# Kernel tuning notes

Measured on AMD Instinct MI355X. Metric: run time of the kernel, lower is better.

Reference implementation:

```python
import jax, jax.numpy as jnp
import numpy as np

CUTOFF = 5.0
NUM_RADIAL = 8
MAX_DEGREE = 3
NUM_EMB = 64
N_ELEM = 83
N_ATOMS = 20000
N_NBR = 32

# degree index for each of the 16 (l,m) components: l=0(x1),1(x3),2(x5),3(x7)
_LM_TO_L = np.repeat(np.arange(MAX_DEGREE + 1), [1, 3, 5, 7])


def jinclike(x, num, limit):
    """Jinc-like radial basis, f_n version (arXiv:1907.02374). x: (...,) -> (..., num)."""
    i = jnp.arange(num, dtype=jnp.float32)
    factor1 = (2.0 ** 0.5) * jnp.pi / (limit ** 1.5)
    factor2 = ((-1.0) ** i) * (i + 1.0) * (i + 2.0) / jnp.hypot(i + 1.0, i + 2.0)
    x = x[..., None]
    return factor1 * factor2 * (jnp.sinc(x / limit * (i + 1.0)) + jnp.sinc(x / limit * (i + 2.0)))


def sph_harm16(u):
    """Real spherical harmonics up to l=3, Racah normalization (Y00=1),
    spherical order m=-l..l (cartesian_order=False). u: (..., 3) unit vectors -> (..., 16)."""
    x, y, z = u[..., 0], u[..., 1], u[..., 2]
    s3, s6, s10, s15 = 3.0 ** 0.5, 6.0 ** 0.5, 10.0 ** 0.5, 15.0 ** 0.5
    one = jnp.ones_like(x)
    comps = [
        one,                                   # l=0
        y, z, x,                               # l=1, m=-1,0,1
        s3 * x * y, s3 * y * z, 0.5 * (3.0 * z * z - 1.0), s3 * x * z, 0.5 * s3 * (x * x - y * y),  # l=2
        0.25 * s10 * y * (3.0 * x * x - y * y), s15 * x * y * z, 0.25 * s6 * y * (5.0 * z * z - 1.0),
        0.5 * z * (5.0 * z * z - 3.0),
        0.25 * s6 * x * (5.0 * z * z - 1.0), 0.5 * s15 * z * (x * x - y * y), 0.25 * s10 * x * (x * x - 3.0 * y * y),  # l=3
    ]
    return jnp.stack(comps, axis=-1)


def setup_inputs() -> dict:
    key = jax.random.key(0)
    k1, k2, k3, k4, k5, k6 = jax.random.split(key, 6)
    neighbour_displacements = 1.5 * jax.random.normal(k1, (N_ATOMS, N_NBR, 3), dtype=jnp.float32)
    Z_j = jax.random.randint(k2, (N_ATOMS, N_NBR), 0, N_ELEM, dtype=jnp.int32)
    embed_table = jax.random.normal(k3, (N_ELEM, NUM_EMB), dtype=jnp.float32)
    dense_w = jax.random.normal(k4, (NUM_EMB, NUM_RADIAL), dtype=jnp.float32) / (NUM_EMB ** 0.5)
    dense_b = 0.01 * jax.random.normal(k5, (NUM_RADIAL,), dtype=jnp.float32)
    tensor_w = jax.random.normal(k6, (MAX_DEGREE + 1, NUM_RADIAL), dtype=jnp.float32)
    return {"neighbour_displacements": neighbour_displacements, "Z_j": Z_j,
            "embed_table": embed_table, "dense_w": dense_w, "dense_b": dense_b,
            "tensor_w": tensor_w}


def reference(neighbour_displacements, Z_j, embed_table, dense_w, dense_b, tensor_w):
    # radial x angular basis expansion: (N, K, 16, 8)
    norm = jnp.linalg.norm(neighbour_displacements, axis=-1)            # (N, K)
    u = neighbour_displacements / norm[..., None]                        # unit vectors
    rbf = jinclike(norm, NUM_RADIAL, CUTOFF)                             # (N, K, 8)
    sh = sph_harm16(u)                                                   # (N, K, 16)
    basis = sh[..., :, None] * rbf[..., None, :]                         # (N, K, 16, 8)

    # species embedding -> dense transform to num_radial channels (scalar, l=0 features)
    emb = embed_table[Z_j]                                               # (N, K, 64)
    t = emb @ dense_w + dense_b                                          # (N, K, 8)

    # CG tensor product with a scalar (l=0) left input collapses exactly to a
    # per-degree weighted elementwise product: y[lm,f] = w[l(lm),f] * t[f] * basis[lm,f]
    wexp = tensor_w[_LM_TO_L]                                            # (16, 8)
    y = wexp * t[..., None, :] * basis                                   # (N, K, 16, 8)

    y = y.at[..., 0, :].add(t)

    return y[..., None, :, :].astype(jnp.float32)
```

## Files before the change

### kernel.cpp

```cpp
#include <hip/hip_runtime.h>
#include <math.h>

#define N_ATOMS   20000
#define N_NBR     32
#define NBR_TOTAL (N_ATOMS * N_NBR)
#define N_ELEM    83
#define NUM_EMB   64
#define NUM_RAD   8

__global__ __launch_bounds__(256) void sarb_kernel(
    const float* __restrict__ disp,
    const int*   __restrict__ Zj,
    const float* __restrict__ embed,
    const float* __restrict__ dw,
    const float* __restrict__ db,
    const float* __restrict__ tw,
    float* __restrict__ out)
{
    __shared__ float Fl[N_ELEM * NUM_RAD];
    __shared__ float lds[256 * 33];

    const int tid = threadIdx.x;

    for (int i = tid; i < N_ELEM * NUM_RAD; i += 256) {
        int z = i >> 3, f = i & 7;
        float acc = db[f];
        const float* er = embed + z * NUM_EMB;
        for (int e = 0; e < NUM_EMB; ++e)
            acc = fmaf(er[e], dw[e * 8 + f], acc);
        Fl[i] = acc;
    }
    __syncthreads();

    const int n = blockIdx.x * 256 + tid;
    const float dx = disp[n * 3 + 0];
    const float dy = disp[n * 3 + 1];
    const float dz = disp[n * 3 + 2];
    const int   z  = Zj[n];

    const float r2  = dx * dx + dy * dy + dz * dz;
    const float nrm = sqrtf(r2);
    const float inv = 1.0f / nrm;
    const float x = dx * inv, y = dy * inv, zu = dz * inv;

    const float s3 = 1.7320508075688772f, s6 = 2.449489742783178f;
    const float s10 = 3.1622776601683795f, s15 = 3.872983346207417f;
    const float x2 = x * x, y2 = y * y, z2 = zu * zu;
    const float xy = x * y, yz = y * zu, xz = x * zu;

    const int base = tid * 33;
    lds[base + 0]  = 1.0f;
    lds[base + 1]  = y;
    lds[base + 2]  = zu;
    lds[base + 3]  = x;
    lds[base + 4]  = s3 * xy;
    lds[base + 5]  = s3 * yz;
    lds[base + 6]  = 0.5f * (3.0f * z2 - 1.0f);
    lds[base + 7]  = s3 * xz;
    lds[base + 8]  = 0.5f * s3 * (x2 - y2);
    lds[base + 9]  = 0.25f * s10 * y * (3.0f * x2 - y2);
    lds[base + 10] = s15 * xy * zu;
    lds[base + 11] = 0.25f * s6 * y * (5.0f * z2 - 1.0f);
    lds[base + 12] = 0.5f * zu * (5.0f * z2 - 3.0f);
    lds[base + 13] = 0.25f * s6 * x * (5.0f * z2 - 1.0f);
    lds[base + 14] = 0.5f * s15 * zu * (x2 - y2);
    lds[base + 15] = 0.25f * s10 * x * (x2 - 3.0f * y2);

    const float a = 0.6283185307179586f * nrm;
    float sv[9];
    {
        const float s1  = sinf(a);
        const float c2  = 2.0f * cosf(a);
        const float inva = 1.0f / a;
        const float invk[9] = {1.0f, 0.5f, 0.33333333f, 0.25f, 0.2f,
                               0.16666667f, 0.14285714f, 0.125f, 0.11111111f};
        float sprev = 0.0f, scur = s1;
        #pragma unroll
        for (int k = 0; k < 9; ++k) {
            sv[k] = scur * inva * invk[k];
            float snext = c2 * scur - sprev;
            sprev = scur; scur = snext;
        }
        if (a < 1e-12f) {
            #pragma unroll
            for (int k = 0; k < 9; ++k) sv[k] = 1.0f;
        }
    }
    #pragma unroll
    for (int i = 0; i < 8; ++i) {
        const float ip1 = (float)(i + 1), ip2 = (float)(i + 2);
        float f2 = ip1 * ip2 / sqrtf(ip1 * ip1 + ip2 * ip2);
        if (i & 1) f2 = -f2;
        const float rbf = 0.3973835397f * f2 * (sv[i] + sv[i + 1]);
        const float tf  = Fl[z * 8 + i];
        lds[base + 16 + i] = tf * rbf;
        lds[base + 24 + i] = tf;
    }
    __syncthreads();

    const int chunk = tid & 31;
    const int lm = chunk >> 1;
    const int fh = (chunk & 1) * 4;
    const int l  = (lm > 0) + (lm > 3) + (lm > 8);
    const float4 wv = *reinterpret_cast<const float4*>(tw + l * 8 + fh);

    float4* outv = reinterpret_cast<float4*>(out) + (size_t)blockIdx.x * 8192;
    const int nb0 = tid >> 5;
    #pragma unroll
    for (int k = 0; k < 32; ++k) {
        const int nb = k * 8 + nb0;
        const int b  = nb * 33;
        const float s = lds[b + lm];
        const float g0 = lds[b + 16 + fh + 0];
        const float g1 = lds[b + 16 + fh + 1];
        const float g2 = lds[b + 16 + fh + 2];
        const float g3 = lds[b + 16 + fh + 3];
        float4 r;
        r.x = wv.x * s * g0;
        r.y = wv.y * s * g1;
        r.z = wv.z * s * g2;
        r.w = wv.w * s * g3;
        if (lm == 0) {
            r.x += lds[b + 24 + fh + 0];
            r.y += lds[b + 24 + fh + 1];
            r.z += lds[b + 24 + fh + 2];
            r.w += lds[b + 24 + fh + 3];
        }
        outv[k * 256 + tid] = r;
    }
}

extern "C" void kernel_launch(void* const* d_in, const int* in_sizes, int n_in,
                              void* d_out, int out_size, void* d_ws, size_t ws_size,
                              hipStream_t stream) {
    const float* disp  = (const float*)d_in[0];
    const int*   Zj    = (const int*)  d_in[1];
    const float* embed = (const float*)d_in[2];
    const float* dw    = (const float*)d_in[3];
    const float* db    = (const float*)d_in[4];
    const float* tw    = (const float*)d_in[5];
    float* out = (float*)d_out;

    sarb_kernel<<<dim3(NBR_TOTAL / 256), dim3(256), 0, stream>>>(
        disp, Zj, embed, dw, db, tw, out);
}
```

Before: 352.0 us.

## Precompute species-to-radial table in separate kernel and streamline output stage

Moves the 83x8 embedding-dense table computation out of every block into a tiny prologue kernel writing to workspace. Each block then only copies the table into padded LDS. The row stride is padded to 34 so LDS reads can be 8-byte vectors. The l=0 residual is folded into a precomputed slot, which removes the branch in the store loop. The change also uses fast __sincosf and nontemporal stores for the large output. The risks are an extra kernel launch and the lower precision of the fast sincos.

```diff
diff --git a/kernel.cpp b/kernel.cpp
--- a/kernel.cpp
+++ b/kernel.cpp
@@ -6,36 +6,46 @@
 #define NBR_TOTAL (N_ATOMS * N_NBR)
 #define N_ELEM    83
 #define NUM_EMB   64
-#define NUM_RAD   8
+#define ROWW      34
+
+typedef float f32x4 __attribute__((ext_vector_type(4)));
+
+__global__ __launch_bounds__(256) void f_table_kernel(
+    const float* __restrict__ embed, const float* __restrict__ dw,
+    const float* __restrict__ db, float* __restrict__ F)
+{
+    const int i = blockIdx.x * 256 + threadIdx.x;
+    if (i < N_ELEM * 8) {
+        const int z = i >> 3, f = i & 7;
+        float acc = db[f];
+        const float* er = embed + z * NUM_EMB;
+        #pragma unroll 8
+        for (int e = 0; e < NUM_EMB; ++e)
+            acc = fmaf(er[e], dw[e * 8 + f], acc);
+        F[i] = acc;
+    }
+}
 
 __global__ __launch_bounds__(256) void sarb_kernel(
     const float* __restrict__ disp,
     const int*   __restrict__ Zj,
-    const float* __restrict__ embed,
-    const float* __restrict__ dw,
-    const float* __restrict__ db,
     const float* __restrict__ tw,
+    const float* __restrict__ Fg,
     float* __restrict__ out)
 {
-    __shared__ float Fl[N_ELEM * NUM_RAD];
-    __shared__ float lds[256 * 33];
+    __shared__ float Fl[N_ELEM * 9 + 1];
+    __shared__ __align__(16) float lds[256 * ROWW];
 
     const int tid = threadIdx.x;
 
-    for (int i = tid; i < N_ELEM * NUM_RAD; i += 256) {
-        int z = i >> 3, f = i & 7;
-        float acc = db[f];
-        const float* er = embed + z * NUM_EMB;
-        for (int e = 0; e < NUM_EMB; ++e)
-            acc = fmaf(er[e], dw[e * 8 + f], acc);
-        Fl[i] = acc;
-    }
+    for (int i = tid; i < N_ELEM * 8; i += 256)
+        Fl[(i >> 3) * 9 + (i & 7)] = Fg[i];
     __syncthreads();
 
     const int n = blockIdx.x * 256 + tid;
-    const float dx = disp[n * 3 + 0];
-    const float dy = disp[n * 3 + 1];
-    const float dz = disp[n * 3 + 2];
+    const float dx = disp[3 * n + 0];
+    const float dy = disp[3 * n + 1];
+    const float dz = disp[3 * n + 2];
     const int   z  = Zj[n];
 
     const float r2  = dx * dx + dy * dy + dz * dz;
@@ -48,37 +58,38 @@
     const float x2 = x * x, y2 = y * y, z2 = zu * zu;
     const float xy = x * y, yz = y * zu, xz = x * zu;
 
-    const int base = tid * 33;
-    lds[base + 0]  = 1.0f;
-    lds[base + 1]  = y;
-    lds[base + 2]  = zu;
-    lds[base + 3]  = x;
-    lds[base + 4]  = s3 * xy;
-    lds[base + 5]  = s3 * yz;
-    lds[base + 6]  = 0.5f * (3.0f * z2 - 1.0f);
-    lds[base + 7]  = s3 * xz;
-    lds[base + 8]  = 0.5f * s3 * (x2 - y2);
-    lds[base + 9]  = 0.25f * s10 * y * (3.0f * x2 - y2);
-    lds[base + 10] = s15 * xy * zu;
-    lds[base + 11] = 0.25f * s6 * y * (5.0f * z2 - 1.0f);
-    lds[base + 12] = 0.5f * zu * (5.0f * z2 - 3.0f);
-    lds[base + 13] = 0.25f * s6 * x * (5.0f * z2 - 1.0f);
-    lds[base + 14] = 0.5f * s15 * zu * (x2 - y2);
-    lds[base + 15] = 0.25f * s10 * x * (x2 - 3.0f * y2);
+    float* row = lds + tid * ROWW;
+    row[0]  = 1.0f;
+    row[1]  = y;
+    row[2]  = zu;
+    row[3]  = x;
+    row[4]  = s3 * xy;
+    row[5]  = s3 * yz;
+    row[6]  = 0.5f * (3.0f * z2 - 1.0f);
+    row[7]  = s3 * xz;
+    row[8]  = 0.5f * s3 * (x2 - y2);
+    row[9]  = 0.25f * s10 * y * (3.0f * x2 - y2);
+    row[10] = s15 * xy * zu;
+    row[11] = 0.25f * s6 * y * (5.0f * z2 - 1.0f);
+    row[12] = 0.5f * zu * (5.0f * z2 - 3.0f);
+    row[13] = 0.25f * s6 * x * (5.0f * z2 - 1.0f);
+    row[14] = 0.5f * s15 * zu * (x2 - y2);
+    row[15] = 0.25f * s10 * x * (x2 - 3.0f * y2);
 
     const float a = 0.6283185307179586f * nrm;
     float sv[9];
     {
-        const float s1  = sinf(a);
-        const float c2  = 2.0f * cosf(a);
+        float s1, c1;
+        __sincosf(a, &s1, &c1);
+        const float c2   = 2.0f * c1;
         const float inva = 1.0f / a;
-        const float invk[9] = {1.0f, 0.5f, 0.33333333f, 0.25f, 0.2f,
-                               0.16666667f, 0.14285714f, 0.125f, 0.11111111f};
+        const float invk[9] = {1.0f, 0.5f, 0.33333334f, 0.25f, 0.2f,
+                               0.16666667f, 0.14285715f, 0.125f, 0.11111111f};
         float sprev = 0.0f, scur = s1;
         #pragma unroll
         for (int k = 0; k < 9; ++k) {
             sv[k] = scur * inva * invk[k];
-            float snext = c2 * scur - sprev;
+            const float snext = c2 * scur - sprev;
             sprev = scur; scur = snext;
         }
         if (a < 1e-12f) {
@@ -92,41 +103,36 @@
         float f2 = ip1 * ip2 / sqrtf(ip1 * ip1 + ip2 * ip2);
         if (i & 1) f2 = -f2;
         const float rbf = 0.3973835397f * f2 * (sv[i] + sv[i + 1]);
-        const float tf  = Fl[z * 8 + i];
-        lds[base + 16 + i] = tf * rbf;
-        lds[base + 24 + i] = tf;
+        const float tf  = Fl[z * 9 + i];
+        row[16 + i] = tf * rbf;
+        row[24 + i] = fmaf(tw[i] * rbf, tf, tf);
     }
     __syncthreads();
 
     const int chunk = tid & 31;
-    const int lm = chunk >> 1;
-    const int fh = (chunk & 1) * 4;
-    const int l  = (lm > 0) + (lm > 3) + (lm > 8);
-    const float4 wv = *reinterpret_cast<const float4*>(tw + l * 8 + fh);
+    const int lm  = chunk >> 1;
+    const int fh4 = chunk & 1;
+    const int l   = (lm > 0) + (lm > 3) + (lm > 8);
+    f32x4 wv;
+    if (lm == 0) { wv = (f32x4){1.0f, 1.0f, 1.0f, 1.0f}; }
+    else         { wv = *reinterpret_cast<const f32x4*>(tw + l * 8 + fh4 * 4); }
+    const int goff = (lm ? 16 : 24) + fh4 * 4;
 
-    float4* outv = reinterpret_cast<float4*>(out) + (size_t)blockIdx.x * 8192;
+    f32x4* __restrict__ outv =
+        reinterpret_cast<f32x4*>(out) + (size_t)blockIdx.x * 8192;
     const int nb0 = tid >> 5;
     #pragma unroll
     for (int k = 0; k < 32; ++k) {
-        const int nb = k * 8 + nb0;
-        const int b  = nb * 33;
-        const float s = lds[b + lm];
-        const float g0 = lds[b + 16 + fh + 0];
-        const float g1 = lds[b + 16 + fh + 1];
-        const float g2 = lds[b + 16 + fh + 2];
-        const float g3 = lds[b + 16 + fh + 3];
-        float4 r;
-        r.x = wv.x * s * g0;
-        r.y = wv.y * s * g1;
-        r.z = wv.z * s * g2;
-        r.w = wv.w * s * g3;
-        if (lm == 0) {
-            r.x += lds[b + 24 + fh + 0];
-            r.y += lds[b + 24 + fh + 1];
-            r.z += lds[b + 24 + fh + 2];
-            r.w += lds[b + 24 + fh + 3];
-        }
-        outv[k * 256 + tid] = r;
+        const int rb = (k * 8 + nb0) * ROWW;
+        const float  s  = lds[rb + lm];
+        const float2 ga = *reinterpret_cast<const float2*>(lds + rb + goff);
+        const float2 gb = *reinterpret_cast<const float2*>(lds + rb + goff + 2);
+        f32x4 r;
+        r.x = wv.x * s * ga.x;
+        r.y = wv.y * s * ga.y;
+        r.z = wv.z * s * gb.x;
+        r.w = wv.w * s * gb.y;
+        __builtin_nontemporal_store(r, outv + k * 256 + tid);
     }
 }
 
@@ -140,7 +146,8 @@
     const float* db    = (const float*)d_in[4];
     const float* tw    = (const float*)d_in[5];
     float* out = (float*)d_out;
+    float* F   = (float*)d_ws;
 
-    sarb_kernel<<<dim3(NBR_TOTAL / 256), dim3(256), 0, stream>>>(
-        disp, Zj, embed, dw, db, tw, out);
+    f_table_kernel<<<dim3(3), dim3(256), 0, stream>>>(embed, dw, db, F);
+    sarb_kernel<<<dim3(NBR_TOTAL / 256), dim3(256), 0, stream>>>(disp, Zj, tw, F, out);
 }
```

New measurement: 344.8 us. -2.0%, faster.
